# Kernel optimization log

Measured on AMD Instinct MI355X. Metric: run time of the kernel, lower is better.

The kernel has to match this reference:

```python
import jax, jax.numpy as jnp
import numpy as np

B, M, D = 8, 1024, 1024
H = 16
HD = D // H  # 64
F = 4096

def layer_norm(x, gamma, beta, eps=1e-5):
    mu = jnp.mean(x, axis=-1, keepdims=True)
    var = jnp.var(x, axis=-1, keepdims=True)
    return (x - mu) * jax.lax.rsqrt(var + eps) * gamma + beta

def setup_inputs() -> dict:
    key = jax.random.key(0)
    ks = jax.random.split(key, 16)
    s = 0.02
    return {
        "h": jax.random.normal(ks[0], (B, M, D), jnp.float32),
        "h_all": jax.random.normal(ks[1], (B, M, D), jnp.float32),
        "Wq": jax.random.normal(ks[2], (D, D), jnp.float32) * s,
        "Wk": jax.random.normal(ks[3], (D, D), jnp.float32) * s,
        "Wv": jax.random.normal(ks[4], (D, D), jnp.float32) * s,
        "Wo": jax.random.normal(ks[5], (D, D), jnp.float32) * s,
        "W1": jax.random.normal(ks[6], (D, F), jnp.float32) * s,
        "b1": jnp.zeros((F,), jnp.float32),
        "W2": jax.random.normal(ks[7], (F, D), jnp.float32) * s,
        "b2": jnp.zeros((D,), jnp.float32),
        "g1": jnp.ones((D,), jnp.float32),
        "be1": jnp.zeros((D,), jnp.float32),
        "g2": jnp.ones((D,), jnp.float32),
        "be2": jnp.zeros((D,), jnp.float32),
    }

def reference(h, h_all, Wq, Wk, Wv, Wo, W1, b1, W2, b2, g1, be1, g2, be2):
    Bx, Mx, Dx = h.shape
    # projections (no bias, per nn.Linear(bias=False))
    q = (h @ Wq).reshape(Bx, Mx, H, HD)        # [B,M,H,hd]
    k = (h_all @ Wk).reshape(Bx, -1, H, HD)    # [B,N,H,hd]
    v = (h_all @ Wv).reshape(Bx, -1, H, HD)
    # attention: scale by sqrt(head_dim) as in SeqAttention(hidden_size=head_dim)
    scores = jnp.einsum('bqhd,bkhd->bhqk', q, k) / jnp.sqrt(jnp.float32(HD))
    attn = jax.nn.softmax(scores, axis=-1)
    ctx = jnp.einsum('bhqk,bkhd->bqhd', attn, v).reshape(Bx, Mx, Dx)
    attn_out = ctx @ Wo
    # post-norm residual 1
    h1 = layer_norm(h + attn_out, g1, be1)
    # FFN
    ff = jax.nn.relu(h1 @ W1 + b1) @ W2 + b2
    # post-norm residual 2
    out = layer_norm(h1 + ff, g2, be2)
    return out
```

## Files before the change

kernel.cpp:

```cpp
#include <hip/hip_runtime.h>
#include <hip/hip_bf16.h>

#define ROWS 8192
#define DD   1024
#define HH   16
#define HD   64
#define FF   4096

typedef __attribute__((ext_vector_type(4))) float f32x4;
typedef __attribute__((ext_vector_type(8))) __bf16 bf16x8;

static __device__ __forceinline__ unsigned short f2bf(float f) {
  unsigned u = __float_as_uint(f);
  u += 0x7fffu + ((u >> 16) & 1u);
  return (unsigned short)(u >> 16);
}

static __device__ __forceinline__ float bf2f(unsigned short u) {
  return __uint_as_float(((unsigned)u) << 16);
}

static __device__ __forceinline__ unsigned cvtpk_bf16(float lo, float hi) {
  unsigned r;
  asm("v_cvt_pk_bf16_f32 %0, %1, %2" : "=v"(r) : "v"(lo), "v"(hi));
  return r;
}

static __device__ __forceinline__ f32x4 mfma16(bf16x8 a, bf16x8 b, f32x4 c) {
  return __builtin_amdgcn_mfma_f32_16x16x32_bf16(a, b, c, 0, 0, 0);
}

#define GLOAD16(gp, lp) __builtin_amdgcn_global_load_lds( \
    (__attribute__((address_space(1))) void*)(gp), \
    (__attribute__((address_space(3))) void*)(lp), 16, 0, 0)

__global__ __launch_bounds__(256) void prep_k(
    const float* __restrict__ h, const float* __restrict__ hall,
    const float* __restrict__ Wq, const float* __restrict__ Wk,
    const float* __restrict__ Wv, const float* __restrict__ Wo,
    const float* __restrict__ W1, const float* __restrict__ W2,
    unsigned short* __restrict__ hb, unsigned short* __restrict__ hab,
    unsigned short* __restrict__ wqt, unsigned short* __restrict__ wkvt,
    unsigned short* __restrict__ wot, unsigned short* __restrict__ w1t,
    unsigned short* __restrict__ w2t) {
  __shared__ float tile[32][33];
  const int bid = blockIdx.x;
  const int tid = threadIdx.x;

  if (bid < 16384) {
    const float* src = (bid < 8192) ? h : hall;
    unsigned short* dst = (bid < 8192) ? hb : hab;
    int i = (bid & 8191) * 256 + tid;
    float4 v = ((const float4*)src)[i];
    ushort4 o;
    o.x = f2bf(v.x); o.y = f2bf(v.y); o.z = f2bf(v.z); o.w = f2bf(v.w);
    ((ushort4*)dst)[i] = o;
    return;
  }

  int r = bid - 16384;
  const float* src; unsigned short* dst; int R, C, bx, by;
  if (r < 4096) {
    int which = r >> 10, idx = r & 1023;
    R = C = 1024; bx = idx & 31; by = idx >> 5;
    if (which == 0) { src = Wq; dst = wqt; }
    else if (which == 1) { src = Wk; dst = wkvt; }
    else if (which == 2) { src = Wv; dst = wkvt + (size_t)DD * DD; }
    else { src = Wo; dst = wot; }
  } else if (r < 8192) {
    int idx = r - 4096;
    R = 1024; C = 4096; bx = idx & 127; by = idx >> 7;
    src = W1; dst = w1t;
  } else {
    int idx = r - 8192;
    R = 4096; C = 1024; bx = idx & 31; by = idx >> 5;
    src = W2; dst = w2t;
  }
  const int tx = tid & 31, ty = tid >> 5;
  #pragma unroll
  for (int i = 0; i < 32; i += 8)
    tile[ty + i][tx] = src[(size_t)(by * 32 + ty + i) * C + bx * 32 + tx];
  __syncthreads();
  #pragma unroll
  for (int i = 0; i < 32; i += 8)
    dst[(size_t)(bx * 32 + ty + i) * R + by * 32 + tx] = f2bf(tile[tx][ty + i]);
}

template <int BM, int MODE, int KS = 1>
__global__ __launch_bounds__(512, 2) void gemm256(
    const unsigned short* __restrict__ A, const unsigned short* __restrict__ BT,
    const float* __restrict__ bias, void* __restrict__ Cout, void* __restrict__ Cout2,
    int Ni, int Ki, int nbx) {
  constexpr int MR = BM / 32;

  const int tid  = threadIdx.x;
  const int lane = tid & 63;
  const int wid  = tid >> 6;
  const int wm   = wid >> 2;
  const int wn   = wid & 3;
  const int lr   = lane & 15;
  const int kq   = lane >> 4;
  const int axor = (lr & 7) << 4;

  const int nwg = gridDim.x;
  const int cpx = nwg >> 3;
  const int wg  = (int)blockIdx.x;
  const int swz = (wg & 7) * cpx + (wg >> 3);
  const int perk = nwg / KS;
  const int kh   = swz / perk;
  const int swzr = swz % perk;
  const int bx = swzr % nbx, by = swzr / nbx;
  const int brow = by * BM, bcol = bx * 256;
  const int Kc   = Ki / KS;
  const int kbase = kh * Kc;

  f32x4 acc[MR][4] = {};
  const int NT = Kc >> 6;

  if constexpr (BM == 256) {
    __shared__ unsigned short As[2 * 256 * 64];
    __shared__ unsigned short Bs[2 * 256 * 64];

    const size_t loff = (size_t)(lane >> 3) * Ki + ((lane & 7) ^ (lane >> 3)) * 8;
    const unsigned short* Ab = A + (size_t)brow * Ki + kbase;
    const unsigned short* Bb = BT + (size_t)bcol * Ki + kbase;

    auto stage2 = [&](int qc, int u, int db) {
      const int ra = ((wid & 4) << 5) + qc * 32 + (wid & 3) * 8;
      GLOAD16(Ab + (size_t)ra * Ki + u * 64 + loff,
              (char*)As + db * 32768 + ra * 128);
      const int rb = qc * 64 + wid * 8;
      GLOAD16(Bb + (size_t)rb * Ki + u * 64 + loff,
              (char*)Bs + db * 32768 + rb * 128);
    };

    #pragma unroll
    for (int qc = 0; qc < 4; ++qc) stage2(qc, 0, 0);
    {
      const int u1 = (1 < NT) ? 1 : NT - 1;
      stage2(0, u1, 1); stage2(1, u1, 1); stage2(2, u1, 1);
    }
    asm volatile("s_waitcnt vmcnt(6)" ::: "memory");
    __builtin_amdgcn_s_barrier();
    __builtin_amdgcn_sched_barrier(0);

    #pragma unroll 1
    for (int t = 0; t < NT; ++t) {
      const int d = t & 1;
      const char* ab = (const char*)As + d * 32768;
      const char* bb = (const char*)Bs + d * 32768;
      bf16x8 bfv[4][2];
      #pragma unroll
      for (int q = 0; q < 4; ++q) {
        bf16x8 af[2][2];
        #pragma unroll
        for (int mm = 0; mm < 2; ++mm)
          #pragma unroll
          for (int ks = 0; ks < 2; ++ks)
            af[mm][ks] = *(const bf16x8*)(ab +
                (wm * 128 + (q * 2 + mm) * 16 + lr) * 128 +
                ((ks * 64 + kq * 16) ^ axor));
        if (q == 0) {
          #pragma unroll
          for (int n = 0; n < 4; ++n)
            #pragma unroll
            for (int ks = 0; ks < 2; ++ks)
              bfv[n][ks] = *(const bf16x8*)(bb +
                  (wn * 64 + n * 16 + lr) * 128 +
                  ((ks * 64 + kq * 16) ^ axor));
        }
        if (q == 0) {
          stage2(3, (t + 1 < NT) ? t + 1 : NT - 1, (t + 1) & 1);
        } else {
          stage2(q - 1, (t + 2 < NT) ? t + 2 : NT - 1, d);
        }
        __builtin_amdgcn_sched_barrier(0);
        __builtin_amdgcn_s_barrier();
        asm volatile("s_waitcnt lgkmcnt(0)" ::: "memory");
        __builtin_amdgcn_sched_barrier(0);
        __builtin_amdgcn_s_setprio(1);
        #pragma unroll
        for (int mm = 0; mm < 2; ++mm)
          #pragma unroll
          for (int n = 0; n < 4; ++n) {
            acc[q * 2 + mm][n] = mfma16(af[mm][0], bfv[n][0], acc[q * 2 + mm][n]);
            acc[q * 2 + mm][n] = mfma16(af[mm][1], bfv[n][1], acc[q * 2 + mm][n]);
          }
        __builtin_amdgcn_s_setprio(0);
        if (q == 3) asm volatile("s_waitcnt vmcnt(6)" ::: "memory");
        __builtin_amdgcn_s_barrier();
        __builtin_amdgcn_sched_barrier(0);
      }
    }
    asm volatile("s_waitcnt vmcnt(0)" ::: "memory");
  } else {
    __shared__ unsigned short As[2][BM * 64];
    __shared__ unsigned short Bs[2][256 * 64];
    const int srow = wid * 8 + (lane >> 3);
    const int scol = ((lane & 7) * 8) ^ ((srow & 7) << 3);
    size_t offA[BM / 64], offB[4];
    #pragma unroll
    for (int L = 0; L < BM / 64; ++L)
      offA[L] = (size_t)(brow + L * 64 + srow) * Ki + kbase + scol;
    #pragma unroll
    for (int L = 0; L < 4; ++L)
      offB[L] = (size_t)(bcol + L * 64 + srow) * Ki + kbase + scol;

    auto stage = [&](int t, int d) {
      #pragma unroll
      for (int L = 0; L < BM / 64; ++L)
        GLOAD16(A + offA[L] + t * 64, (char*)As[d] + L * 8192 + wid * 1024);
      #pragma unroll
      for (int L = 0; L < 4; ++L)
        GLOAD16(BT + offB[L] + t * 64, (char*)Bs[d] + L * 8192 + wid * 1024);
    };

    stage(0, 0);
    stage(1, 1);

    #pragma unroll 1
    for (int t = 0; t < NT; ++t) {
      const int d = t & 1;
      asm volatile("s_waitcnt vmcnt(6)" ::: "memory");
      __builtin_amdgcn_s_barrier();
      __builtin_amdgcn_sched_barrier(0);

      const unsigned short* as = As[d];
      const unsigned short* bs = Bs[d];
      #pragma unroll
      for (int kk = 0; kk < 2; ++kk) {
        bf16x8 af[MR], bfv[4];
        #pragma unroll
        for (int m = 0; m < MR; ++m)
          af[m] = *(const bf16x8*)((const char*)as +
              (wm * (BM / 2) + m * 16 + lr) * 128 + ((kk * 64 + kq * 16) ^ axor));
        #pragma unroll
        for (int n = 0; n < 4; ++n)
          bfv[n] = *(const bf16x8*)((const char*)bs +
              (wn * 64 + n * 16 + lr) * 128 + ((kk * 64 + kq * 16) ^ axor));
        #pragma unroll
        for (int m = 0; m < MR; ++m)
          #pragma unroll
          for (int n = 0; n < 4; ++n)
            acc[m][n] = mfma16(af[m], bfv[n], acc[m][n]);
      }

      asm volatile("s_waitcnt lgkmcnt(0)" ::: "memory");
      __builtin_amdgcn_s_barrier();
      __builtin_amdgcn_sched_barrier(0);
      const int ts = (t + 2 < NT) ? t + 2 : NT - 1;
      stage(ts, d);
    }
  }

  #pragma unroll
  for (int m = 0; m < MR; ++m) {
    #pragma unroll
    for (int n = 0; n < 4; ++n) {
      const int r0 = brow + wm * (BM / 2) + m * 16 + kq * 4;
      const int c  = bcol + wn * 64 + n * 16 + lr;
      if constexpr (MODE == 4) {
        if (c < 1024) {
          #pragma unroll
          for (int e = 0; e < 4; ++e)
            ((unsigned short*)Cout)[(size_t)(r0 + e) * 1024 + c] = f2bf(acc[m][n][e]);
        } else {
          const int cc = c - 1024;
          const int bq = r0 >> 10;
          const int tok = r0 & 1023;
          ushort4 pk;
          pk.x = f2bf(acc[m][n][0]); pk.y = f2bf(acc[m][n][1]);
          pk.z = f2bf(acc[m][n][2]); pk.w = f2bf(acc[m][n][3]);
          *(ushort4*)((unsigned short*)Cout2 + ((size_t)bq * 1024 + cc) * 1024 + tok) = pk;
        }
      } else if constexpr (MODE == 5) {
        if (kh == 0) {
          const float bv = bias[c];
          #pragma unroll
          for (int e = 0; e < 4; ++e)
            ((float*)Cout)[(size_t)(r0 + e) * Ni + c] = acc[m][n][e] + bv;
        } else {
          #pragma unroll
          for (int e = 0; e < 4; ++e)
            ((unsigned short*)Cout2)[(size_t)(r0 + e) * Ni + c] = f2bf(acc[m][n][e]);
        }
      } else {
        const float bv = (MODE == 2 || MODE == 3) ? bias[c] : 0.0f;
        #pragma unroll
        for (int e = 0; e < 4; ++e) {
          float v = acc[m][n][e] + bv;
          if (MODE == 2) v = fmaxf(v, 0.0f);
          if (MODE == 0 || MODE == 2)
            ((unsigned short*)Cout)[(size_t)(r0 + e) * Ni + c] = f2bf(v);
          else
            ((float*)Cout)[(size_t)(r0 + e) * Ni + c] = v;
        }
      }
    }
  }
}

__global__ __launch_bounds__(512, 6) void attn_k(
    const unsigned short* __restrict__ q, const unsigned short* __restrict__ k,
    const unsigned short* __restrict__ vT, unsigned short* __restrict__ ctx) {
  __shared__ unsigned short Ks[2][64 * 64];
  __shared__ unsigned short Vt[2][64 * 64];
  __shared__ unsigned short Ps[8][16 * 64];
  const int tid = threadIdx.x;
  const int lane = tid & 63;
  const int wid = tid >> 6;
  const int bh = blockIdx.x;
  const int b = bh >> 4, h = bh & 15;
  const int qrow0 = blockIdx.y * 128 + wid * 16;
  const size_t tokbase = (size_t)b * 1024;
  const int lr = lane & 15, kq = lane >> 4;

  const int srow = tid >> 3;
  const int scol = ((tid & 7) * 8) ^ ((srow & 7) << 3);
  const unsigned short* kg = k + (tokbase + srow) * 1024 + h * 64 + scol;
  const unsigned short* vg = vT + ((size_t)(b * 16 + h) * 64 + srow) * 1024 + scol;
  const int ldst = tid * 16;

  auto stage = [&](int kt, int d) {
    GLOAD16(kg + (size_t)kt * 64 * 1024, (char*)Ks[d] + ldst);
    GLOAD16(vg + kt * 64, (char*)Vt[d] + ldst);
  };

  bf16x8 aq[2];
  {
    const unsigned short* qp = q + (tokbase + qrow0 + lr) * DD + h * 64 + kq * 8;
    aq[0] = *(const bf16x8*)qp;
    aq[1] = *(const bf16x8*)(qp + 32);
  }

  float l_acc = 0.f;
  f32x4 acc[4] = {};
  const float C = 0.125f * 1.4426950408889634f;
  const unsigned swp = (unsigned)((lr & 7) << 4);
  const unsigned pbase = (unsigned)(lr * 128);

  stage(0, 0);
  stage(1, 1);

  #pragma unroll 2
  for (int kt = 0; kt < 16; ++kt) {
    const int d = kt & 1;
    asm volatile("s_waitcnt vmcnt(2)" ::: "memory");
    __builtin_amdgcn_s_barrier();
    __builtin_amdgcn_sched_barrier(0);

    f32x4 sv[4] = {};
    #pragma unroll
    for (int jb = 0; jb < 4; ++jb)
      #pragma unroll
      for (int ks = 0; ks < 2; ++ks) {
        int row = jb * 16 + lr;
        bf16x8 ak = *(const bf16x8*)((const char*)Ks[d] +
            row * 128 + ((ks * 64 + kq * 16) ^ ((row & 7) << 4)));
        sv[jb] = mfma16(ak, aq[ks], sv[jb]);
      }

    #pragma unroll
    for (int jb = 0; jb < 4; ++jb) {
      float p0 = exp2f(sv[jb][0] * C);
      float p1 = exp2f(sv[jb][1] * C);
      float p2 = exp2f(sv[jb][2] * C);
      float p3 = exp2f(sv[jb][3] * C);
      l_acc += (p0 + p1) + (p2 + p3);
      uint2 w;
      w.x = cvtpk_bf16(p0, p1);
      w.y = cvtpk_bf16(p2, p3);
      unsigned off = pbase + (((unsigned)(jb * 32 + kq * 8)) ^ swp);
      *(uint2*)((char*)Ps[wid] + off) = w;
    }

    #pragma unroll
    for (int ks = 0; ks < 2; ++ks) {
      bf16x8 ap = *(const bf16x8*)((const char*)Ps[wid] +
          lr * 128 + ((ks * 64 + kq * 16) ^ ((lr & 7) << 4)));
      #pragma unroll
      for (int db = 0; db < 4; ++db) {
        int dd = db * 16 + lr;
        bf16x8 bv = *(const bf16x8*)((const char*)Vt[d] +
            dd * 128 + ((ks * 64 + kq * 16) ^ ((dd & 7) << 4)));
        acc[db] = mfma16(bv, ap, acc[db]);
      }
    }

    asm volatile("s_waitcnt lgkmcnt(0)" ::: "memory");
    __builtin_amdgcn_s_barrier();
    __builtin_amdgcn_sched_barrier(0);
    const int ts = (kt + 2 < 16) ? kt + 2 : 15;
    stage(ts, d);
  }

  float l = l_acc + __shfl_xor(l_acc, 16);
  l += __shfl_xor(l, 32);
  const float inv = 1.0f / l;
  unsigned short* cp = ctx + (tokbase + qrow0 + lr) * DD + h * 64 + kq * 4;
  #pragma unroll
  for (int db = 0; db < 4; ++db) {
    ushort4 o;
    o.x = f2bf(acc[db][0] * inv);
    o.y = f2bf(acc[db][1] * inv);
    o.z = f2bf(acc[db][2] * inv);
    o.w = f2bf(acc[db][3] * inv);
    *(ushort4*)(cp + db * 16) = o;
  }
}

__global__ __launch_bounds__(256) void ln_add_bb_k(
    const unsigned short* __restrict__ a, const unsigned short* __restrict__ b,
    const float* __restrict__ gamma, const float* __restrict__ beta,
    unsigned short* __restrict__ outb) {
  int row = blockIdx.x;
  int tid = threadIdx.x;
  size_t base = (size_t)row * 1024 + tid * 4;
  ushort4 va = *(const ushort4*)(a + base);
  ushort4 vb = *(const ushort4*)(b + base);
  float x[4] = {bf2f(va.x) + bf2f(vb.x), bf2f(va.y) + bf2f(vb.y),
                bf2f(va.z) + bf2f(vb.z), bf2f(va.w) + bf2f(vb.w)};
  float s = x[0] + x[1] + x[2] + x[3];
  float sq = x[0] * x[0] + x[1] * x[1] + x[2] * x[2] + x[3] * x[3];
  #pragma unroll
  for (int mk = 1; mk < 64; mk <<= 1) {
    s += __shfl_xor(s, mk);
    sq += __shfl_xor(sq, mk);
  }
  __shared__ float red[8];
  int wid = tid >> 6, lane = tid & 63;
  if (lane == 0) { red[wid] = s; red[4 + wid] = sq; }
  __syncthreads();
  s = red[0] + red[1] + red[2] + red[3];
  sq = red[4] + red[5] + red[6] + red[7];
  float mu = s * (1.0f / 1024.0f);
  float var = sq * (1.0f / 1024.0f) - mu * mu;
  float rs = rsqrtf(var + 1e-5f);
  float4 g = *(const float4*)(gamma + tid * 4);
  float4 be = *(const float4*)(beta + tid * 4);
  ushort4 ob;
  ob.x = f2bf((x[0] - mu) * rs * g.x + be.x);
  ob.y = f2bf((x[1] - mu) * rs * g.y + be.y);
  ob.z = f2bf((x[2] - mu) * rs * g.z + be.z);
  ob.w = f2bf((x[3] - mu) * rs * g.w + be.w);
  *(ushort4*)(outb + base) = ob;
}

__global__ __launch_bounds__(256) void ln3_k(
    const unsigned short* __restrict__ a, const float* __restrict__ b,
    const unsigned short* __restrict__ c,
    const float* __restrict__ gamma, const float* __restrict__ beta,
    float* __restrict__ outf) {
  int row = blockIdx.x;
  int tid = threadIdx.x;
  size_t base = (size_t)row * 1024 + tid * 4;
  ushort4 va = *(const ushort4*)(a + base);
  float4 vb = *(const float4*)(b + base);
  ushort4 vc = *(const ushort4*)(c + base);
  float x[4] = {bf2f(va.x) + vb.x + bf2f(vc.x), bf2f(va.y) + vb.y + bf2f(vc.y),
                bf2f(va.z) + vb.z + bf2f(vc.z), bf2f(va.w) + vb.w + bf2f(vc.w)};
  float s = x[0] + x[1] + x[2] + x[3];
  float sq = x[0] * x[0] + x[1] * x[1] + x[2] * x[2] + x[3] * x[3];
  #pragma unroll
  for (int mk = 1; mk < 64; mk <<= 1) {
    s += __shfl_xor(s, mk);
    sq += __shfl_xor(sq, mk);
  }
  __shared__ float red[8];
  int wid = tid >> 6, lane = tid & 63;
  if (lane == 0) { red[wid] = s; red[4 + wid] = sq; }
  __syncthreads();
  s = red[0] + red[1] + red[2] + red[3];
  sq = red[4] + red[5] + red[6] + red[7];
  float mu = s * (1.0f / 1024.0f);
  float var = sq * (1.0f / 1024.0f) - mu * mu;
  float rs = rsqrtf(var + 1e-5f);
  float4 g = *(const float4*)(gamma + tid * 4);
  float4 be = *(const float4*)(beta + tid * 4);
  float4 o;
  o.x = (x[0] - mu) * rs * g.x + be.x;
  o.y = (x[1] - mu) * rs * g.y + be.y;
  o.z = (x[2] - mu) * rs * g.z + be.z;
  o.w = (x[3] - mu) * rs * g.w + be.w;
  *(float4*)(outf + base) = o;
}

extern "C" void kernel_launch(void* const* d_in, const int* in_sizes, int n_in,
                              void* d_out, int out_size, void* d_ws, size_t ws_size,
                              hipStream_t stream) {
  const float* h    = (const float*)d_in[0];
  const float* hall = (const float*)d_in[1];
  const float* Wq   = (const float*)d_in[2];
  const float* Wk   = (const float*)d_in[3];
  const float* Wv   = (const float*)d_in[4];
  const float* Wo   = (const float*)d_in[5];
  const float* W1   = (const float*)d_in[6];
  const float* b1   = (const float*)d_in[7];
  const float* W2   = (const float*)d_in[8];
  const float* b2   = (const float*)d_in[9];
  const float* g1   = (const float*)d_in[10];
  const float* be1  = (const float*)d_in[11];
  const float* g2   = (const float*)d_in[12];
  const float* be2  = (const float*)d_in[13];

  char* ws = (char*)d_ws;
  size_t off = 0;
  auto alloc = [&](size_t n) { size_t o = off; off += (n + 255) & ~(size_t)255; return o; };
  const size_t hb_o   = alloc((size_t)ROWS * DD * 2);
  const size_t hab_o  = alloc((size_t)ROWS * DD * 2);
  const size_t wqt_o  = alloc((size_t)DD * DD * 2);
  const size_t wkvt_o = alloc((size_t)DD * DD * 4);
  const size_t wot_o  = alloc((size_t)DD * DD * 2);
  const size_t w1t_o  = alloc((size_t)DD * FF * 2);
  const size_t w2t_o  = alloc((size_t)FF * DD * 2);
  const size_t qb_o   = alloc((size_t)ROWS * DD * 2);
  const size_t kb_o   = alloc((size_t)ROWS * DD * 2);
  const size_t vt_o   = alloc((size_t)ROWS * DD * 2);
  const size_t cx_o   = alloc((size_t)ROWS * DD * 2);
  const size_t h1b_o  = alloc((size_t)ROWS * DD * 2);
  const size_t fp1_o  = alloc((size_t)ROWS * DD * 2);

  unsigned short* hb   = (unsigned short*)(ws + hb_o);
  unsigned short* hab  = (unsigned short*)(ws + hab_o);
  unsigned short* wqt  = (unsigned short*)(ws + wqt_o);
  unsigned short* wkvt = (unsigned short*)(ws + wkvt_o);
  unsigned short* wot  = (unsigned short*)(ws + wot_o);
  unsigned short* w1t  = (unsigned short*)(ws + w1t_o);
  unsigned short* w2t  = (unsigned short*)(ws + w2t_o);
  unsigned short* qb   = (unsigned short*)(ws + qb_o);
  unsigned short* kb   = (unsigned short*)(ws + kb_o);
  unsigned short* vTb  = (unsigned short*)(ws + vt_o);
  unsigned short* cxb  = (unsigned short*)(ws + cx_o);
  unsigned short* h1b  = (unsigned short*)(ws + h1b_o);
  unsigned short* fp1b = (unsigned short*)(ws + fp1_o);
  unsigned short* attn_ob = (unsigned short*)(ws + hab_o);
  unsigned short* ff1     = (unsigned short*)(ws + qb_o);
  float*          outf    = (float*)d_out;

  prep_k<<<dim3(16384 + 4096 + 4096 + 4096), 256, 0, stream>>>(
      h, hall, Wq, Wk, Wv, Wo, W1, W2, hb, hab, wqt, wkvt, wot, w1t, w2t);

  gemm256<128, 0><<<dim3(256), 512, 0, stream>>>(hb,  wqt,  nullptr, qb, nullptr, DD,   DD, 4);
  gemm256<256, 4><<<dim3(256), 512, 0, stream>>>(hab, wkvt, nullptr, kb, vTb,    2048, DD, 8);

  attn_k<<<dim3(128, 8), 512, 0, stream>>>(qb, kb, vTb, cxb);

  gemm256<128, 0><<<dim3(256), 512, 0, stream>>>(cxb, wot, nullptr, attn_ob, nullptr, DD, DD, 4);
  ln_add_bb_k<<<ROWS, 256, 0, stream>>>(hb, attn_ob, g1, be1, h1b);

  gemm256<256, 2>   <<<dim3(512), 512, 0, stream>>>(h1b, w1t, b1, ff1, nullptr, FF, DD, 16);
  gemm256<256, 5, 2><<<dim3(256), 512, 0, stream>>>(ff1, w2t, b2, outf, fp1b, DD, FF, 4);

  ln3_k<<<ROWS, 256, 0, stream>>>(h1b, outf, fp1b, g2, be2, outf);
}
```

Before: 352.7 us.

## Use 32x32x16 MFMA tiles in the 256-row GEMM path and raise attention MFMA priority

The BM=256 GEMM path switches from 16x16x32 bf16 MFMA to 32x32x16 MFMA. Fragment loads from the swizzled LDS tiles and the epilogue are rewritten to match the 32x32 accumulator layout. The larger instruction needs fewer LDS fragment reads per FLOP and fewer MFMA issues. In exchange it uses a different register layout and scatters epilogue stores more widely. Separately, the attention kernel wraps its QK and PV MFMA blocks in s_setprio so waves interleave better with the softmax work.

```diff
diff --git a/kernel.cpp b/kernel.cpp
--- a/kernel.cpp
+++ b/kernel.cpp
@@ -8,6 +8,7 @@
 #define FF   4096
 
 typedef __attribute__((ext_vector_type(4))) float f32x4;
+typedef __attribute__((ext_vector_type(16))) float f32x16;
 typedef __attribute__((ext_vector_type(8))) __bf16 bf16x8;
 
 static __device__ __forceinline__ unsigned short f2bf(float f) {
@@ -28,6 +29,10 @@
 
 static __device__ __forceinline__ f32x4 mfma16(bf16x8 a, bf16x8 b, f32x4 c) {
   return __builtin_amdgcn_mfma_f32_16x16x32_bf16(a, b, c, 0, 0, 0);
+}
+
+static __device__ __forceinline__ f32x16 mfma32(bf16x8 a, bf16x8 b, f32x16 c) {
+  return __builtin_amdgcn_mfma_f32_32x32x16_bf16(a, b, c, 0, 0, 0);
 }
 
 #define GLOAD16(gp, lp) __builtin_amdgcn_global_load_lds( \
@@ -114,7 +119,6 @@
   const int Kc   = Ki / KS;
   const int kbase = kh * Kc;
 
-  f32x4 acc[MR][4] = {};
   const int NT = Kc >> 6;
 
   if constexpr (BM == 256) {
@@ -144,30 +148,32 @@
     __builtin_amdgcn_s_barrier();
     __builtin_amdgcn_sched_barrier(0);
 
+    const int l31 = lane & 31;
+    const int kh2 = lane >> 5;
+    f32x16 acc32[4][2] = {};
+
     #pragma unroll 1
     for (int t = 0; t < NT; ++t) {
       const int d = t & 1;
       const char* ab = (const char*)As + d * 32768;
       const char* bb = (const char*)Bs + d * 32768;
-      bf16x8 bfv[4][2];
+      bf16x8 bfv[2][4];
       #pragma unroll
       for (int q = 0; q < 4; ++q) {
-        bf16x8 af[2][2];
+        bf16x8 af[4];
         #pragma unroll
-        for (int mm = 0; mm < 2; ++mm)
-          #pragma unroll
-          for (int ks = 0; ks < 2; ++ks)
-            af[mm][ks] = *(const bf16x8*)(ab +
-                (wm * 128 + (q * 2 + mm) * 16 + lr) * 128 +
-                ((ks * 64 + kq * 16) ^ axor));
+        for (int ks = 0; ks < 4; ++ks)
+          af[ks] = *(const bf16x8*)(ab +
+              (wm * 128 + q * 32 + l31) * 128 +
+              (((ks * 2 + kh2) ^ (l31 & 7)) << 4));
         if (q == 0) {
           #pragma unroll
-          for (int n = 0; n < 4; ++n)
+          for (int ng = 0; ng < 2; ++ng)
             #pragma unroll
-            for (int ks = 0; ks < 2; ++ks)
-              bfv[n][ks] = *(const bf16x8*)(bb +
-                  (wn * 64 + n * 16 + lr) * 128 +
-                  ((ks * 64 + kq * 16) ^ axor));
+            for (int ks = 0; ks < 4; ++ks)
+              bfv[ng][ks] = *(const bf16x8*)(bb +
+                  (wn * 64 + ng * 32 + l31) * 128 +
+                  (((ks * 2 + kh2) ^ (l31 & 7)) << 4));
         }
         if (q == 0) {
           stage2(3, (t + 1 < NT) ? t + 1 : NT - 1, (t + 1) & 1);
@@ -180,12 +186,10 @@
         __builtin_amdgcn_sched_barrier(0);
         __builtin_amdgcn_s_setprio(1);
         #pragma unroll
-        for (int mm = 0; mm < 2; ++mm)
+        for (int ng = 0; ng < 2; ++ng)
           #pragma unroll
-          for (int n = 0; n < 4; ++n) {
-            acc[q * 2 + mm][n] = mfma16(af[mm][0], bfv[n][0], acc[q * 2 + mm][n]);
-            acc[q * 2 + mm][n] = mfma16(af[mm][1], bfv[n][1], acc[q * 2 + mm][n]);
-          }
+          for (int ks = 0; ks < 4; ++ks)
+            acc32[q][ng] = mfma32(af[ks], bfv[ng][ks], acc32[q][ng]);
         __builtin_amdgcn_s_setprio(0);
         if (q == 3) asm volatile("s_waitcnt vmcnt(6)" ::: "memory");
         __builtin_amdgcn_s_barrier();
@@ -193,6 +197,65 @@
       }
     }
     asm volatile("s_waitcnt vmcnt(0)" ::: "memory");
+
+    #pragma unroll
+    for (int mg = 0; mg < 4; ++mg) {
+      #pragma unroll
+      for (int ng = 0; ng < 2; ++ng) {
+        const int c = bcol + wn * 64 + ng * 32 + l31;
+        const int rb0 = brow + wm * 128 + mg * 32 + kh2 * 4;
+        if constexpr (MODE == 4) {
+          if (c < 1024) {
+            #pragma unroll
+            for (int g = 0; g < 4; ++g)
+              #pragma unroll
+              for (int e = 0; e < 4; ++e)
+                ((unsigned short*)Cout)[(size_t)(rb0 + 8 * g + e) * 1024 + c] =
+                    f2bf(acc32[mg][ng][g * 4 + e]);
+          } else {
+            const int cc = c - 1024;
+            #pragma unroll
+            for (int g = 0; g < 4; ++g) {
+              const int r0 = rb0 + 8 * g;
+              const int bq = r0 >> 10, tok = r0 & 1023;
+              ushort4 pk;
+              pk.x = f2bf(acc32[mg][ng][g * 4 + 0]);
+              pk.y = f2bf(acc32[mg][ng][g * 4 + 1]);
+              pk.z = f2bf(acc32[mg][ng][g * 4 + 2]);
+              pk.w = f2bf(acc32[mg][ng][g * 4 + 3]);
+              *(ushort4*)((unsigned short*)Cout2 +
+                          ((size_t)bq * 1024 + cc) * 1024 + tok) = pk;
+            }
+          }
+        } else if constexpr (MODE == 5) {
+          if (kh == 0) {
+            const float bv = bias[c];
+            #pragma unroll
+            for (int g = 0; g < 4; ++g)
+              #pragma unroll
+              for (int e = 0; e < 4; ++e)
+                ((float*)Cout)[(size_t)(rb0 + 8 * g + e) * Ni + c] =
+                    acc32[mg][ng][g * 4 + e] + bv;
+          } else {
+            #pragma unroll
+            for (int g = 0; g < 4; ++g)
+              #pragma unroll
+              for (int e = 0; e < 4; ++e)
+                ((unsigned short*)Cout2)[(size_t)(rb0 + 8 * g + e) * Ni + c] =
+                    f2bf(acc32[mg][ng][g * 4 + e]);
+          }
+        } else {
+          const float bv = bias[c];
+          #pragma unroll
+          for (int g = 0; g < 4; ++g)
+            #pragma unroll
+            for (int e = 0; e < 4; ++e) {
+              float v = fmaxf(acc32[mg][ng][g * 4 + e] + bv, 0.0f);
+              ((unsigned short*)Cout)[(size_t)(rb0 + 8 * g + e) * Ni + c] = f2bf(v);
+            }
+        }
+      }
+    }
   } else {
     __shared__ unsigned short As[2][BM * 64];
     __shared__ unsigned short Bs[2][256 * 64];
@@ -214,6 +277,8 @@
       for (int L = 0; L < 4; ++L)
         GLOAD16(BT + offB[L] + t * 64, (char*)Bs[d] + L * 8192 + wid * 1024);
     };
+
+    f32x4 acc[MR][4] = {};
 
     stage(0, 0);
     stage(1, 1);
@@ -251,40 +316,13 @@
       const int ts = (t + 2 < NT) ? t + 2 : NT - 1;
       stage(ts, d);
     }
-  }
-
-  #pragma unroll
-  for (int m = 0; m < MR; ++m) {
-    #pragma unroll
-    for (int n = 0; n < 4; ++n) {
-      const int r0 = brow + wm * (BM / 2) + m * 16 + kq * 4;
-      const int c  = bcol + wn * 64 + n * 16 + lr;
-      if constexpr (MODE == 4) {
-        if (c < 1024) {
-          #pragma unroll
-          for (int e = 0; e < 4; ++e)
-            ((unsigned short*)Cout)[(size_t)(r0 + e) * 1024 + c] = f2bf(acc[m][n][e]);
-        } else {
-          const int cc = c - 1024;
-          const int bq = r0 >> 10;
-          const int tok = r0 & 1023;
-          ushort4 pk;
-          pk.x = f2bf(acc[m][n][0]); pk.y = f2bf(acc[m][n][1]);
-          pk.z = f2bf(acc[m][n][2]); pk.w = f2bf(acc[m][n][3]);
-          *(ushort4*)((unsigned short*)Cout2 + ((size_t)bq * 1024 + cc) * 1024 + tok) = pk;
-        }
-      } else if constexpr (MODE == 5) {
-        if (kh == 0) {
-          const float bv = bias[c];
-          #pragma unroll
-          for (int e = 0; e < 4; ++e)
-            ((float*)Cout)[(size_t)(r0 + e) * Ni + c] = acc[m][n][e] + bv;
-        } else {
-          #pragma unroll
-          for (int e = 0; e < 4; ++e)
-            ((unsigned short*)Cout2)[(size_t)(r0 + e) * Ni + c] = f2bf(acc[m][n][e]);
-        }
-      } else {
+
+    #pragma unroll
+    for (int m = 0; m < MR; ++m) {
+      #pragma unroll
+      for (int n = 0; n < 4; ++n) {
+        const int r0 = brow + wm * (BM / 2) + m * 16 + kq * 4;
+        const int c  = bcol + wn * 64 + n * 16 + lr;
         const float bv = (MODE == 2 || MODE == 3) ? bias[c] : 0.0f;
         #pragma unroll
         for (int e = 0; e < 4; ++e) {
@@ -350,6 +388,7 @@
     __builtin_amdgcn_sched_barrier(0);
 
     f32x4 sv[4] = {};
+    __builtin_amdgcn_s_setprio(1);
     #pragma unroll
     for (int jb = 0; jb < 4; ++jb)
       #pragma unroll
@@ -359,6 +398,7 @@
             row * 128 + ((ks * 64 + kq * 16) ^ ((row & 7) << 4)));
         sv[jb] = mfma16(ak, aq[ks], sv[jb]);
       }
+    __builtin_amdgcn_s_setprio(0);
 
     #pragma unroll
     for (int jb = 0; jb < 4; ++jb) {
@@ -374,6 +414,7 @@
       *(uint2*)((char*)Ps[wid] + off) = w;
     }
 
+    __builtin_amdgcn_s_setprio(1);
     #pragma unroll
     for (int ks = 0; ks < 2; ++ks) {
       bf16x8 ap = *(const bf16x8*)((const char*)Ps[wid] +
@@ -386,6 +427,7 @@
         acc[db] = mfma16(bv, ap, acc[db]);
       }
     }
+    __builtin_amdgcn_s_setprio(0);
 
     asm volatile("s_waitcnt lgkmcnt(0)" ::: "memory");
     __builtin_amdgcn_s_barrier();
```

Result: slower. 363.9 us (+3.2%).
